# Optimization experiments

Measured on AMD Instinct MI355X. Metric: run time of the kernel, lower is better.

The kernel has to match this reference:

```python
import jax, jax.numpy as jnp
import numpy as np

N = 10000
E = 320000
F_IN = 512
NHID = 32
LATENT = 16


def setup_inputs() -> dict:
    key = jax.random.key(0)
    k1, k2, k3, k4, k5 = jax.random.split(key, 5)
    x = jax.random.normal(k1, (N, F_IN), dtype=jnp.float32)
    W1 = jax.random.normal(k2, (F_IN, NHID), dtype=jnp.float32) * (1.0 / np.sqrt(F_IN))
    W2 = jax.random.normal(k3, (NHID, LATENT), dtype=jnp.float32) * (1.0 / np.sqrt(NHID))
    edge_index = jax.random.randint(k4, (2, E), 0, N, dtype=jnp.int32)
    edge_weight = jax.random.uniform(k5, (E,), dtype=jnp.float32)
    return {"x": x, "W1": W1, "W2": W2, "edge_index": edge_index,
            "edge_weight": edge_weight}


def _spmm(edge_index, edge_weight, h):
    # out[dst] += w * h[src]  (sparse normalized-adjacency matmul)
    src, dst = edge_index[0], edge_index[1]
    msgs = edge_weight[:, None] * h[src]          # [E, D] gather + scale
    return jax.ops.segment_sum(msgs, dst, num_segments=N)  # [N, D]


def reference(x, W1, W2, edge_index, edge_weight):
    # GCNConv layer 1: adj @ (x @ W1)
    h = _spmm(edge_index, edge_weight, x @ W1)    # [N, NHID]
    # GCNConv layer 2: adj @ (h @ W2)
    z = _spmm(edge_index, edge_weight, h @ W2)    # [N, LATENT]
    # Inner-product decoder: sigmoid(z @ z^T)
    adj_recon = jax.nn.sigmoid(z @ z.T)           # [N, N]
    return adj_recon, z
```

## Files before the change

kernel.cpp:

```cpp
#include <hip/hip_runtime.h>
#include <cstdint>
#include <cstddef>

#define N_NODES 10000
#define F_IN    512
#define NHID    32
#define LATENT  16

__global__ __launch_bounds__(256) void gemm1_kernel(const float* __restrict__ x,
                                                    const float* __restrict__ W1,
                                                    float* __restrict__ h0) {
    __shared__ float xs[8][F_IN];
    const int row0 = blockIdx.x * 8;
    for (int t = threadIdx.x; t < 8 * F_IN; t += 256) {
        const int r = t >> 9;
        const int c = t & (F_IN - 1);
        if (row0 + r < N_NODES)
            xs[r][c] = x[(size_t)(row0 + r) * F_IN + c];
    }
    __syncthreads();

    const int col = threadIdx.x & 31;
    const int r   = threadIdx.x >> 5;
    if (row0 + r < N_NODES) {
        float acc = 0.f;
#pragma unroll 8
        for (int k = 0; k < F_IN; ++k) {
            acc += xs[r][k] * W1[k * NHID + col];
        }
        h0[(size_t)(row0 + r) * NHID + col] = acc;
    }
}

template <int D>
__global__ __launch_bounds__(256) void spmm_kernel(const int* __restrict__ src,
                                                   const int* __restrict__ dst,
                                                   const float* __restrict__ w,
                                                   const float* __restrict__ hin,
                                                   float* __restrict__ hout,
                                                   int E) {
    const int idx = blockIdx.x * 256 + threadIdx.x;
    const int e = idx / D;
    const int d = idx & (D - 1);
    if (e < E) {
        const int s = src[e];
        const int t = dst[e];
        const float val = w[e] * hin[(size_t)s * D + d];
        atomicAdd(&hout[(size_t)t * D + d], val);
    }
}

__global__ __launch_bounds__(256) void gemm2_kernel(const float* __restrict__ h,
                                                    const float* __restrict__ W2,
                                                    float* __restrict__ z0) {
    __shared__ float w2s[NHID * LATENT];
    for (int t = threadIdx.x; t < NHID * LATENT; t += 256) w2s[t] = W2[t];
    __syncthreads();

    const int idx = blockIdx.x * 256 + threadIdx.x;
    if (idx < N_NODES * LATENT) {
        const int row = idx >> 4;
        const int col = idx & (LATENT - 1);
        const float* __restrict__ hr = h + (size_t)row * NHID;
        float acc = 0.f;
#pragma unroll
        for (int k = 0; k < NHID; ++k) acc += hr[k] * w2s[k * LATENT + col];
        z0[idx] = acc;
    }
}

#define TI 32

__device__ __forceinline__ float sigmoid_fast(float x) {
    return __builtin_amdgcn_rcpf(1.0f + __expf(-x));
}

__global__ __launch_bounds__(256) void decoder_kernel(const float* __restrict__ z,
                                                      float* __restrict__ out) {
    const int j  = blockIdx.x * 256 + threadIdx.x;
    const int i0 = blockIdx.y * TI;

    float4 zj0, zj1, zj2, zj3;
    if (j < N_NODES) {
        const float4* __restrict__ zp = (const float4*)(z + (size_t)j * LATENT);
        zj0 = zp[0]; zj1 = zp[1]; zj2 = zp[2]; zj3 = zp[3];
    } else {
        zj0 = zj1 = zj2 = zj3 = make_float4(0.f, 0.f, 0.f, 0.f);
    }

    const int imax = min(TI, N_NODES - i0);
    if (imax == TI) {
#pragma unroll 4
        for (int ii = 0; ii < TI; ++ii) {
            const float4* __restrict__ zi = (const float4*)(z + (size_t)(i0 + ii) * LATENT);
            const float4 a0 = zi[0], a1 = zi[1], a2 = zi[2], a3 = zi[3];
            float acc = a0.x * zj0.x + a0.y * zj0.y + a0.z * zj0.z + a0.w * zj0.w
                      + a1.x * zj1.x + a1.y * zj1.y + a1.z * zj1.z + a1.w * zj1.w
                      + a2.x * zj2.x + a2.y * zj2.y + a2.z * zj2.z + a2.w * zj2.w
                      + a3.x * zj3.x + a3.y * zj3.y + a3.z * zj3.z + a3.w * zj3.w;
            if (j < N_NODES) {
                __builtin_nontemporal_store(sigmoid_fast(acc),
                                            &out[(size_t)(i0 + ii) * N_NODES + j]);
            }
        }
    } else {
        for (int ii = 0; ii < imax; ++ii) {
            const float4* __restrict__ zi = (const float4*)(z + (size_t)(i0 + ii) * LATENT);
            const float4 a0 = zi[0], a1 = zi[1], a2 = zi[2], a3 = zi[3];
            float acc = a0.x * zj0.x + a0.y * zj0.y + a0.z * zj0.z + a0.w * zj0.w
                      + a1.x * zj1.x + a1.y * zj1.y + a1.z * zj1.z + a1.w * zj1.w
                      + a2.x * zj2.x + a2.y * zj2.y + a2.z * zj2.z + a2.w * zj2.w
                      + a3.x * zj3.x + a3.y * zj3.y + a3.z * zj3.z + a3.w * zj3.w;
            if (j < N_NODES) {
                __builtin_nontemporal_store(sigmoid_fast(acc),
                                            &out[(size_t)(i0 + ii) * N_NODES + j]);
            }
        }
    }
}

extern "C" void kernel_launch(void* const* d_in, const int* in_sizes, int n_in,
                              void* d_out, int out_size, void* d_ws, size_t ws_size,
                              hipStream_t stream) {
    const float* x  = (const float*)d_in[0];
    const float* W1 = (const float*)d_in[1];
    const float* W2 = (const float*)d_in[2];
    const int*   ei = (const int*)d_in[3];
    const float* ew = (const float*)d_in[4];
    const int E = in_sizes[3] / 2;
    const int* src = ei;
    const int* dst = ei + E;

    float* out = (float*)d_out;
    float* z   = out + (size_t)N_NODES * N_NODES;

    float* h0 = out;
    float* h  = h0 + N_NODES * NHID;
    float* z0 = h  + N_NODES * NHID;

    hipMemsetAsync(h, 0, (size_t)N_NODES * NHID * sizeof(float), stream);
    hipMemsetAsync(z, 0, (size_t)N_NODES * LATENT * sizeof(float), stream);

    gemm1_kernel<<<(N_NODES + 7) / 8, 256, 0, stream>>>(x, W1, h0);
    spmm_kernel<NHID><<<(E * NHID + 255) / 256, 256, 0, stream>>>(src, dst, ew, h0, h, E);

    gemm2_kernel<<<(N_NODES * LATENT + 255) / 256, 256, 0, stream>>>(h, W2, z0);
    spmm_kernel<LATENT><<<(E * LATENT + 255) / 256, 256, 0, stream>>>(src, dst, ew, z0, z, E);

    dim3 dgrid((N_NODES + 255) / 256, (N_NODES + TI - 1) / TI);
    decoder_kernel<<<dgrid, 256, 0, stream>>>(z, out);
}
```

Before: 511.8 us.

## Build CSR by destination, replace atomic SpMM with gather, retune GEMMs and decoder

Adds a histogram, a single-block scan and a scatter pass that build a destination-sorted CSR of (src, weight) pairs on every call. Both SpMM layers become per-node gather reductions instead of per-edge atomicAdd scatters. Separately, gemm1 is restructured to stage W1 in shared memory and use float4 accumulation, gemm2 uses vectorized loads, and the decoder computes two columns per thread with TI=40 and 64-bit nontemporal stores. The CSR build adds extra kernels, atomics and a serial scan. Edges with the same destination are placed in nondeterministic order, so floating-point sums are not bitwise reproducible.

```diff
diff --git a/kernel.cpp b/kernel.cpp
--- a/kernel.cpp
+++ b/kernel.cpp
@@ -7,47 +7,133 @@
 #define NHID    32
 #define LATENT  16
 
+typedef float v2f __attribute__((ext_vector_type(2)));
+
+#define OF_H0   0
+#define OF_H    320000
+#define OF_Z0   640000
+#define OF_DEG  800000
+#define OF_RP   810240
+#define OF_CUR  820496
+#define OF_ESW  830752
+
+__global__ __launch_bounds__(256) void hist_kernel(const int* __restrict__ dst,
+                                                   int* __restrict__ deg, int E) {
+    const int e = blockIdx.x * 256 + threadIdx.x;
+    if (e < E) atomicAdd(&deg[dst[e]], 1);
+}
+
+__global__ __launch_bounds__(1024) void scan_kernel(const int* __restrict__ deg,
+                                                    int* __restrict__ row_ptr,
+                                                    int* __restrict__ cursor) {
+    __shared__ int sums[1024];
+    const int tid = threadIdx.x;
+    const int base = tid * 10;
+    int local[10];
+    int s = 0;
+#pragma unroll
+    for (int i = 0; i < 10; ++i) { local[i] = s; s += deg[base + i]; }
+    sums[tid] = s;
+    __syncthreads();
+    for (int off = 1; off < 1024; off <<= 1) {
+        int v = (tid >= off) ? sums[tid - off] : 0;
+        __syncthreads();
+        sums[tid] += v;
+        __syncthreads();
+    }
+    const int excl = (tid == 0) ? 0 : sums[tid - 1];
+#pragma unroll
+    for (int i = 0; i < 10; ++i) {
+        const int g = base + i;
+        if (g <= N_NODES) {
+            const int rp = excl + local[i];
+            row_ptr[g] = rp;
+            cursor[g]  = rp;
+        }
+    }
+}
+
+__global__ __launch_bounds__(256) void scatter_kernel(const int* __restrict__ src,
+                                                      const int* __restrict__ dst,
+                                                      const float* __restrict__ w,
+                                                      int* __restrict__ cursor,
+                                                      int2* __restrict__ esw, int E) {
+    const int e = blockIdx.x * 256 + threadIdx.x;
+    if (e < E) {
+        const int d = dst[e];
+        const int pos = atomicAdd(&cursor[d], 1);
+        esw[pos] = make_int2(src[e], __float_as_int(w[e]));
+    }
+}
+
+#define G1_KC 256
 __global__ __launch_bounds__(256) void gemm1_kernel(const float* __restrict__ x,
                                                     const float* __restrict__ W1,
                                                     float* __restrict__ h0) {
-    __shared__ float xs[8][F_IN];
-    const int row0 = blockIdx.x * 8;
-    for (int t = threadIdx.x; t < 8 * F_IN; t += 256) {
-        const int r = t >> 9;
-        const int c = t & (F_IN - 1);
-        if (row0 + r < N_NODES)
-            xs[r][c] = x[(size_t)(row0 + r) * F_IN + c];
-    }
-    __syncthreads();
-
-    const int col = threadIdx.x & 31;
-    const int r   = threadIdx.x >> 5;
-    if (row0 + r < N_NODES) {
-        float acc = 0.f;
-#pragma unroll 8
-        for (int k = 0; k < F_IN; ++k) {
-            acc += xs[r][k] * W1[k * NHID + col];
-        }
-        h0[(size_t)(row0 + r) * NHID + col] = acc;
+    __shared__ float w1s[G1_KC * NHID];
+    const int row0 = blockIdx.x * 32;
+    const int rp   = threadIdx.x >> 3;
+    const int cg   = (threadIdx.x & 7) * 4;
+    const int gr   = min(row0 + rp, N_NODES - 1);
+    const float4* __restrict__ xrow = (const float4*)(x + (size_t)gr * F_IN);
+
+    float4 acc = make_float4(0.f, 0.f, 0.f, 0.f);
+
+    for (int kc = 0; kc < F_IN; kc += G1_KC) {
+        {
+            const float4* __restrict__ wg = (const float4*)(W1 + (size_t)kc * NHID);
+            float4* __restrict__ ws4 = (float4*)w1s;
+            const int b = threadIdx.x * 8;
+#pragma unroll
+            for (int i = 0; i < 8; ++i) ws4[b + i] = wg[b + i];
+        }
+        __syncthreads();
+
+        const int k4base = kc >> 2;
+#pragma unroll 4
+        for (int kk4 = 0; kk4 < G1_KC / 4; ++kk4) {
+            const float4 xv = xrow[k4base + kk4];
+            const float4 w0 = *(const float4*)&w1s[(kk4 * 4 + 0) * NHID + cg];
+            const float4 w1 = *(const float4*)&w1s[(kk4 * 4 + 1) * NHID + cg];
+            const float4 w2 = *(const float4*)&w1s[(kk4 * 4 + 2) * NHID + cg];
+            const float4 w3 = *(const float4*)&w1s[(kk4 * 4 + 3) * NHID + cg];
+            acc.x += xv.x * w0.x + xv.y * w1.x + xv.z * w2.x + xv.w * w3.x;
+            acc.y += xv.x * w0.y + xv.y * w1.y + xv.z * w2.y + xv.w * w3.y;
+            acc.z += xv.x * w0.z + xv.y * w1.z + xv.z * w2.z + xv.w * w3.z;
+            acc.w += xv.x * w0.w + xv.y * w1.w + xv.z * w2.w + xv.w * w3.w;
+        }
+        __syncthreads();
+    }
+
+    if (row0 + rp < N_NODES) {
+        *(float4*)&h0[(size_t)(row0 + rp) * NHID + cg] = acc;
     }
 }
 
 template <int D>
-__global__ __launch_bounds__(256) void spmm_kernel(const int* __restrict__ src,
-                                                   const int* __restrict__ dst,
-                                                   const float* __restrict__ w,
-                                                   const float* __restrict__ hin,
-                                                   float* __restrict__ hout,
-                                                   int E) {
+__global__ __launch_bounds__(256) void gather_kernel(const int* __restrict__ row_ptr,
+                                                     const int2* __restrict__ esw,
+                                                     const float* __restrict__ hin,
+                                                     float* __restrict__ hout) {
     const int idx = blockIdx.x * 256 + threadIdx.x;
-    const int e = idx / D;
+    const int n = idx / D;
     const int d = idx & (D - 1);
-    if (e < E) {
-        const int s = src[e];
-        const int t = dst[e];
-        const float val = w[e] * hin[(size_t)s * D + d];
-        atomicAdd(&hout[(size_t)t * D + d], val);
-    }
+    if (n >= N_NODES) return;
+    const int beg = row_ptr[n];
+    const int end = row_ptr[n + 1];
+    float acc = 0.f;
+    int p = beg;
+    for (; p + 1 < end; p += 2) {
+        const int2 e0 = esw[p];
+        const int2 e1 = esw[p + 1];
+        acc += __int_as_float(e0.y) * hin[(size_t)e0.x * D + d];
+        acc += __int_as_float(e1.y) * hin[(size_t)e1.x * D + d];
+    }
+    if (p < end) {
+        const int2 e0 = esw[p];
+        acc += __int_as_float(e0.y) * hin[(size_t)e0.x * D + d];
+    }
+    hout[(size_t)n * D + d] = acc;
 }
 
 __global__ __launch_bounds__(256) void gemm2_kernel(const float* __restrict__ h,
@@ -61,15 +147,21 @@
     if (idx < N_NODES * LATENT) {
         const int row = idx >> 4;
         const int col = idx & (LATENT - 1);
-        const float* __restrict__ hr = h + (size_t)row * NHID;
+        const float4* __restrict__ hr = (const float4*)(h + (size_t)row * NHID);
         float acc = 0.f;
 #pragma unroll
-        for (int k = 0; k < NHID; ++k) acc += hr[k] * w2s[k * LATENT + col];
+        for (int k4 = 0; k4 < NHID / 4; ++k4) {
+            const float4 hv = hr[k4];
+            acc += hv.x * w2s[(k4 * 4 + 0) * LATENT + col]
+                 + hv.y * w2s[(k4 * 4 + 1) * LATENT + col]
+                 + hv.z * w2s[(k4 * 4 + 2) * LATENT + col]
+                 + hv.w * w2s[(k4 * 4 + 3) * LATENT + col];
+        }
         z0[idx] = acc;
     }
 }
 
-#define TI 32
+#define TI 40
 
 __device__ __forceinline__ float sigmoid_fast(float x) {
     return __builtin_amdgcn_rcpf(1.0f + __expf(-x));
@@ -77,44 +169,37 @@
 
 __global__ __launch_bounds__(256) void decoder_kernel(const float* __restrict__ z,
                                                       float* __restrict__ out) {
-    const int j  = blockIdx.x * 256 + threadIdx.x;
+    const int j0 = (blockIdx.x * 256 + threadIdx.x) * 2;
     const int i0 = blockIdx.y * TI;
 
-    float4 zj0, zj1, zj2, zj3;
-    if (j < N_NODES) {
-        const float4* __restrict__ zp = (const float4*)(z + (size_t)j * LATENT);
-        zj0 = zp[0]; zj1 = zp[1]; zj2 = zp[2]; zj3 = zp[3];
+    float4 a0, a1, a2, a3, b0, b1, b2, b3;
+    if (j0 < N_NODES) {
+        const float4* __restrict__ zp = (const float4*)(z + (size_t)j0 * LATENT);
+        a0 = zp[0]; a1 = zp[1]; a2 = zp[2]; a3 = zp[3];
+        b0 = zp[4]; b1 = zp[5]; b2 = zp[6]; b3 = zp[7];
     } else {
-        zj0 = zj1 = zj2 = zj3 = make_float4(0.f, 0.f, 0.f, 0.f);
-    }
-
-    const int imax = min(TI, N_NODES - i0);
-    if (imax == TI) {
+        a0 = a1 = a2 = a3 = make_float4(0.f, 0.f, 0.f, 0.f);
+        b0 = b1 = b2 = b3 = a0;
+    }
+
 #pragma unroll 4
-        for (int ii = 0; ii < TI; ++ii) {
-            const float4* __restrict__ zi = (const float4*)(z + (size_t)(i0 + ii) * LATENT);
-            const float4 a0 = zi[0], a1 = zi[1], a2 = zi[2], a3 = zi[3];
-            float acc = a0.x * zj0.x + a0.y * zj0.y + a0.z * zj0.z + a0.w * zj0.w
-                      + a1.x * zj1.x + a1.y * zj1.y + a1.z * zj1.z + a1.w * zj1.w
-                      + a2.x * zj2.x + a2.y * zj2.y + a2.z * zj2.z + a2.w * zj2.w
-                      + a3.x * zj3.x + a3.y * zj3.y + a3.z * zj3.z + a3.w * zj3.w;
-            if (j < N_NODES) {
-                __builtin_nontemporal_store(sigmoid_fast(acc),
-                                            &out[(size_t)(i0 + ii) * N_NODES + j]);
-            }
-        }
-    } else {
-        for (int ii = 0; ii < imax; ++ii) {
-            const float4* __restrict__ zi = (const float4*)(z + (size_t)(i0 + ii) * LATENT);
-            const float4 a0 = zi[0], a1 = zi[1], a2 = zi[2], a3 = zi[3];
-            float acc = a0.x * zj0.x + a0.y * zj0.y + a0.z * zj0.z + a0.w * zj0.w
-                      + a1.x * zj1.x + a1.y * zj1.y + a1.z * zj1.z + a1.w * zj1.w
-                      + a2.x * zj2.x + a2.y * zj2.y + a2.z * zj2.z + a2.w * zj2.w
-                      + a3.x * zj3.x + a3.y * zj3.y + a3.z * zj3.z + a3.w * zj3.w;
-            if (j < N_NODES) {
-                __builtin_nontemporal_store(sigmoid_fast(acc),
-                                            &out[(size_t)(i0 + ii) * N_NODES + j]);
-            }
+    for (int ii = 0; ii < TI; ++ii) {
+        const int i = i0 + ii;
+        const float4* __restrict__ zi = (const float4*)(z + (size_t)i * LATENT);
+        const float4 c0 = zi[0], c1 = zi[1], c2 = zi[2], c3 = zi[3];
+        const float s0 = c0.x * a0.x + c0.y * a0.y + c0.z * a0.z + c0.w * a0.w
+                       + c1.x * a1.x + c1.y * a1.y + c1.z * a1.z + c1.w * a1.w
+                       + c2.x * a2.x + c2.y * a2.y + c2.z * a2.z + c2.w * a2.w
+                       + c3.x * a3.x + c3.y * a3.y + c3.z * a3.z + c3.w * a3.w;
+        const float s1 = c0.x * b0.x + c0.y * b0.y + c0.z * b0.z + c0.w * b0.w
+                       + c1.x * b1.x + c1.y * b1.y + c1.z * b1.z + c1.w * b1.w
+                       + c2.x * b2.x + c2.y * b2.y + c2.z * b2.z + c2.w * b2.w
+                       + c3.x * b3.x + c3.y * b3.y + c3.z * b3.z + c3.w * b3.w;
+        if (j0 < N_NODES) {
+            v2f r;
+            r.x = sigmoid_fast(s0);
+            r.y = sigmoid_fast(s1);
+            __builtin_nontemporal_store(r, (v2f*)(out + (size_t)i * N_NODES + j0));
         }
     }
 }
@@ -134,19 +219,25 @@
     float* out = (float*)d_out;
     float* z   = out + (size_t)N_NODES * N_NODES;
 
-    float* h0 = out;
-    float* h  = h0 + N_NODES * NHID;
-    float* z0 = h  + N_NODES * NHID;
-
-    hipMemsetAsync(h, 0, (size_t)N_NODES * NHID * sizeof(float), stream);
-    hipMemsetAsync(z, 0, (size_t)N_NODES * LATENT * sizeof(float), stream);
-
-    gemm1_kernel<<<(N_NODES + 7) / 8, 256, 0, stream>>>(x, W1, h0);
-    spmm_kernel<NHID><<<(E * NHID + 255) / 256, 256, 0, stream>>>(src, dst, ew, h0, h, E);
+    float* h0     = out + OF_H0;
+    float* h      = out + OF_H;
+    float* z0     = out + OF_Z0;
+    int*   deg    = (int*)(out + OF_DEG);
+    int*   rowp   = (int*)(out + OF_RP);
+    int*   cursor = (int*)(out + OF_CUR);
+    int2*  esw    = (int2*)(out + OF_ESW);
+
+    hipMemsetAsync(deg, 0, 10240 * sizeof(int), stream);
+    hist_kernel<<<(E + 255) / 256, 256, 0, stream>>>(dst, deg, E);
+    scan_kernel<<<1, 1024, 0, stream>>>(deg, rowp, cursor);
+    scatter_kernel<<<(E + 255) / 256, 256, 0, stream>>>(src, dst, ew, cursor, esw, E);
+
+    gemm1_kernel<<<(N_NODES + 31) / 32, 256, 0, stream>>>(x, W1, h0);
+    gather_kernel<NHID><<<(N_NODES * NHID + 255) / 256, 256, 0, stream>>>(rowp, esw, h0, h);
 
     gemm2_kernel<<<(N_NODES * LATENT + 255) / 256, 256, 0, stream>>>(h, W2, z0);
-    spmm_kernel<LATENT><<<(E * LATENT + 255) / 256, 256, 0, stream>>>(src, dst, ew, z0, z, E);
-
-    dim3 dgrid((N_NODES + 255) / 256, (N_NODES + TI - 1) / TI);
+    gather_kernel<LATENT><<<(N_NODES * LATENT + 255) / 256, 256, 0, stream>>>(rowp, esw, z0, z);
+
+    dim3 dgrid((N_NODES / 2 + 255) / 256, N_NODES / TI);
     decoder_kernel<<<dgrid, 256, 0, stream>>>(z, out);
 }
```

After: 529.2 us. +3.4%, slower.

## Fuse memset into GEMM1, fuse GEMM2 into SpMM2, vectorize decoder stores

Applied to the files above, without the earlier changes.

The two memsets are folded into a combined stage-1 kernel that computes x@W1 with W1 staged in shared memory and float4 outputs, while extra blocks zero the accumulators. The second layer's dense projection is fused into the SpMM, so each edge computes h[src]@W2 on the fly. This removes the z0 buffer and a launch but repeats the 32x16 projection per edge. The decoder now computes 4 columns per thread with 128-bit nontemporal stores and TI=40, dropping the tail-handling branch. It relies on N being divisible by 4 and by 40.

```diff
diff --git a/kernel.cpp b/kernel.cpp
--- a/kernel.cpp
+++ b/kernel.cpp
@@ -7,69 +7,123 @@
 #define NHID    32
 #define LATENT  16
 
-__global__ __launch_bounds__(256) void gemm1_kernel(const float* __restrict__ x,
-                                                    const float* __restrict__ W1,
-                                                    float* __restrict__ h0) {
-    __shared__ float xs[8][F_IN];
-    const int row0 = blockIdx.x * 8;
-    for (int t = threadIdx.x; t < 8 * F_IN; t += 256) {
-        const int r = t >> 9;
-        const int c = t & (F_IN - 1);
-        if (row0 + r < N_NODES)
-            xs[r][c] = x[(size_t)(row0 + r) * F_IN + c];
+typedef float v4f __attribute__((ext_vector_type(4)));
+
+#define OF_H0   0
+#define OF_H    320000
+
+#define G1_TILES 313
+#define ZERO_BLOCKS 64
+#define G1_KC 256
+
+__global__ __launch_bounds__(256) void stage1_kernel(const float* __restrict__ x,
+                                                     const float* __restrict__ W1,
+                                                     float* __restrict__ h0,
+                                                     float* __restrict__ h,
+                                                     float* __restrict__ z) {
+    __shared__ float w1s[G1_KC * NHID];
+
+    if (blockIdx.x >= G1_TILES) {
+        const int tid = (blockIdx.x - G1_TILES) * 256 + threadIdx.x;
+        const int nthr = ZERO_BLOCKS * 256;
+        float4* __restrict__ h4 = (float4*)h;
+        float4* __restrict__ z4 = (float4*)z;
+        const v4f zero = {0.f, 0.f, 0.f, 0.f};
+        for (int i = tid; i < (N_NODES * NHID) / 4; i += nthr)
+            *(v4f*)&h4[i] = zero;
+        for (int i = tid; i < (N_NODES * LATENT) / 4; i += nthr)
+            *(v4f*)&z4[i] = zero;
+        return;
     }
-    __syncthreads();
 
-    const int col = threadIdx.x & 31;
-    const int r   = threadIdx.x >> 5;
-    if (row0 + r < N_NODES) {
-        float acc = 0.f;
-#pragma unroll 8
-        for (int k = 0; k < F_IN; ++k) {
-            acc += xs[r][k] * W1[k * NHID + col];
+    const int row0 = blockIdx.x * 32;
+    const int rp   = threadIdx.x >> 3;
+    const int cg   = (threadIdx.x & 7) * 4;
+    const int gr   = min(row0 + rp, N_NODES - 1);
+    const float4* __restrict__ xrow = (const float4*)(x + (size_t)gr * F_IN);
+
+    float4 acc = make_float4(0.f, 0.f, 0.f, 0.f);
+
+    for (int kc = 0; kc < F_IN; kc += G1_KC) {
+        {
+            const float4* __restrict__ wg = (const float4*)(W1 + (size_t)kc * NHID);
+            float4* __restrict__ ws4 = (float4*)w1s;
+            const int b = threadIdx.x * 8;
+#pragma unroll
+            for (int i = 0; i < 8; ++i) ws4[b + i] = wg[b + i];
         }
-        h0[(size_t)(row0 + r) * NHID + col] = acc;
+        __syncthreads();
+
+        const int k4base = kc >> 2;
+#pragma unroll 4
+        for (int kk4 = 0; kk4 < G1_KC / 4; ++kk4) {
+            const float4 xv = xrow[k4base + kk4];
+            const float4 w0 = *(const float4*)&w1s[(kk4 * 4 + 0) * NHID + cg];
+            const float4 w1 = *(const float4*)&w1s[(kk4 * 4 + 1) * NHID + cg];
+            const float4 w2 = *(const float4*)&w1s[(kk4 * 4 + 2) * NHID + cg];
+            const float4 w3 = *(const float4*)&w1s[(kk4 * 4 + 3) * NHID + cg];
+            acc.x += xv.x * w0.x + xv.y * w1.x + xv.z * w2.x + xv.w * w3.x;
+            acc.y += xv.x * w0.y + xv.y * w1.y + xv.z * w2.y + xv.w * w3.y;
+            acc.z += xv.x * w0.z + xv.y * w1.z + xv.z * w2.z + xv.w * w3.z;
+            acc.w += xv.x * w0.w + xv.y * w1.w + xv.z * w2.w + xv.w * w3.w;
+        }
+        __syncthreads();
+    }
+
+    if (row0 + rp < N_NODES) {
+        *(float4*)&h0[(size_t)(row0 + rp) * NHID + cg] = acc;
     }
 }
 
-template <int D>
-__global__ __launch_bounds__(256) void spmm_kernel(const int* __restrict__ src,
-                                                   const int* __restrict__ dst,
-                                                   const float* __restrict__ w,
-                                                   const float* __restrict__ hin,
-                                                   float* __restrict__ hout,
-                                                   int E) {
+__global__ __launch_bounds__(256) void spmm32_kernel(const int* __restrict__ src,
+                                                     const int* __restrict__ dst,
+                                                     const float* __restrict__ w,
+                                                     const float* __restrict__ hin,
+                                                     float* __restrict__ hout,
+                                                     int E) {
     const int idx = blockIdx.x * 256 + threadIdx.x;
-    const int e = idx / D;
-    const int d = idx & (D - 1);
+    const int e = idx >> 5;
+    const int d = idx & 31;
     if (e < E) {
         const int s = src[e];
         const int t = dst[e];
-        const float val = w[e] * hin[(size_t)s * D + d];
-        atomicAdd(&hout[(size_t)t * D + d], val);
+        const float val = w[e] * hin[(size_t)s * NHID + d];
+        atomicAdd(&hout[(size_t)t * NHID + d], val);
     }
 }
 
-__global__ __launch_bounds__(256) void gemm2_kernel(const float* __restrict__ h,
-                                                    const float* __restrict__ W2,
-                                                    float* __restrict__ z0) {
+__global__ __launch_bounds__(256) void l2_fused_kernel(const int* __restrict__ src,
+                                                       const int* __restrict__ dst,
+                                                       const float* __restrict__ w,
+                                                       const float* __restrict__ h,
+                                                       const float* __restrict__ W2,
+                                                       float* __restrict__ z,
+                                                       int E) {
     __shared__ float w2s[NHID * LATENT];
     for (int t = threadIdx.x; t < NHID * LATENT; t += 256) w2s[t] = W2[t];
     __syncthreads();
 
     const int idx = blockIdx.x * 256 + threadIdx.x;
-    if (idx < N_NODES * LATENT) {
-        const int row = idx >> 4;
-        const int col = idx & (LATENT - 1);
-        const float* __restrict__ hr = h + (size_t)row * NHID;
+    const int e = idx >> 4;
+    const int d = idx & (LATENT - 1);
+    if (e < E) {
+        const int s = src[e];
+        const int t = dst[e];
+        const float4* __restrict__ hr = (const float4*)(h + (size_t)s * NHID);
         float acc = 0.f;
 #pragma unroll
-        for (int k = 0; k < NHID; ++k) acc += hr[k] * w2s[k * LATENT + col];
-        z0[idx] = acc;
+        for (int k4 = 0; k4 < NHID / 4; ++k4) {
+            const float4 hv = hr[k4];
+            acc += hv.x * w2s[(k4 * 4 + 0) * LATENT + d]
+                 + hv.y * w2s[(k4 * 4 + 1) * LATENT + d]
+                 + hv.z * w2s[(k4 * 4 + 2) * LATENT + d]
+                 + hv.w * w2s[(k4 * 4 + 3) * LATENT + d];
+        }
+        atomicAdd(&z[(size_t)t * LATENT + d], w[e] * acc);
     }
 }
 
-#define TI 32
+#define TI 40
 
 __device__ __forceinline__ float sigmoid_fast(float x) {
     return __builtin_amdgcn_rcpf(1.0f + __expf(-x));
@@ -77,45 +131,35 @@
 
 __global__ __launch_bounds__(256) void decoder_kernel(const float* __restrict__ z,
                                                       float* __restrict__ out) {
-    const int j  = blockIdx.x * 256 + threadIdx.x;
+    const int j0 = (blockIdx.x * 256 + threadIdx.x) * 4;
     const int i0 = blockIdx.y * TI;
+    if (j0 >= N_NODES) return;
 
-    float4 zj0, zj1, zj2, zj3;
-    if (j < N_NODES) {
-        const float4* __restrict__ zp = (const float4*)(z + (size_t)j * LATENT);
-        zj0 = zp[0]; zj1 = zp[1]; zj2 = zp[2]; zj3 = zp[3];
-    } else {
-        zj0 = zj1 = zj2 = zj3 = make_float4(0.f, 0.f, 0.f, 0.f);
+    float4 zj[4][4];
+    {
+        const float4* __restrict__ zp = (const float4*)(z + (size_t)j0 * LATENT);
+#pragma unroll
+        for (int c = 0; c < 4; ++c)
+#pragma unroll
+            for (int q = 0; q < 4; ++q) zj[c][q] = zp[c * 4 + q];
     }
 
-    const int imax = min(TI, N_NODES - i0);
-    if (imax == TI) {
-#pragma unroll 4
-        for (int ii = 0; ii < TI; ++ii) {
-            const float4* __restrict__ zi = (const float4*)(z + (size_t)(i0 + ii) * LATENT);
-            const float4 a0 = zi[0], a1 = zi[1], a2 = zi[2], a3 = zi[3];
-            float acc = a0.x * zj0.x + a0.y * zj0.y + a0.z * zj0.z + a0.w * zj0.w
-                      + a1.x * zj1.x + a1.y * zj1.y + a1.z * zj1.z + a1.w * zj1.w
-                      + a2.x * zj2.x + a2.y * zj2.y + a2.z * zj2.z + a2.w * zj2.w
-                      + a3.x * zj3.x + a3.y * zj3.y + a3.z * zj3.z + a3.w * zj3.w;
-            if (j < N_NODES) {
-                __builtin_nontemporal_store(sigmoid_fast(acc),
-                                            &out[(size_t)(i0 + ii) * N_NODES + j]);
-            }
+#pragma unroll 2
+    for (int ii = 0; ii < TI; ++ii) {
+        const int i = i0 + ii;
+        const float4* __restrict__ zi = (const float4*)(z + (size_t)i * LATENT);
+        const float4 c0 = zi[0], c1 = zi[1], c2 = zi[2], c3 = zi[3];
+        v4f r;
+#pragma unroll
+        for (int c = 0; c < 4; ++c) {
+            const float s =
+                  c0.x * zj[c][0].x + c0.y * zj[c][0].y + c0.z * zj[c][0].z + c0.w * zj[c][0].w
+                + c1.x * zj[c][1].x + c1.y * zj[c][1].y + c1.z * zj[c][1].z + c1.w * zj[c][1].w
+                + c2.x * zj[c][2].x + c2.y * zj[c][2].y + c2.z * zj[c][2].z + c2.w * zj[c][2].w
+                + c3.x * zj[c][3].x + c3.y * zj[c][3].y + c3.z * zj[c][3].z + c3.w * zj[c][3].w;
+            r[c] = sigmoid_fast(s);
         }
-    } else {
-        for (int ii = 0; ii < imax; ++ii) {
-            const float4* __restrict__ zi = (const float4*)(z + (size_t)(i0 + ii) * LATENT);
-            const float4 a0 = zi[0], a1 = zi[1], a2 = zi[2], a3 = zi[3];
-            float acc = a0.x * zj0.x + a0.y * zj0.y + a0.z * zj0.z + a0.w * zj0.w
-                      + a1.x * zj1.x + a1.y * zj1.y + a1.z * zj1.z + a1.w * zj1.w
-                      + a2.x * zj2.x + a2.y * zj2.y + a2.z * zj2.z + a2.w * zj2.w
-                      + a3.x * zj3.x + a3.y * zj3.y + a3.z * zj3.z + a3.w * zj3.w;
-            if (j < N_NODES) {
-                __builtin_nontemporal_store(sigmoid_fast(acc),
-                                            &out[(size_t)(i0 + ii) * N_NODES + j]);
-            }
-        }
+        __builtin_nontemporal_store(r, (v4f*)(out + (size_t)i * N_NODES + j0));
     }
 }
 
@@ -133,20 +177,15 @@
 
     float* out = (float*)d_out;
     float* z   = out + (size_t)N_NODES * N_NODES;
+    float* h0  = out + OF_H0;
+    float* h   = out + OF_H;
 
-    float* h0 = out;
-    float* h  = h0 + N_NODES * NHID;
-    float* z0 = h  + N_NODES * NHID;
+    stage1_kernel<<<G1_TILES + ZERO_BLOCKS, 256, 0, stream>>>(x, W1, h0, h, z);
 
-    hipMemsetAsync(h, 0, (size_t)N_NODES * NHID * sizeof(float), stream);
-    hipMemsetAsync(z, 0, (size_t)N_NODES * LATENT * sizeof(float), stream);
+    spmm32_kernel<<<(E * NHID + 255) / 256, 256, 0, stream>>>(src, dst, ew, h0, h, E);
 
-    gemm1_kernel<<<(N_NODES + 7) / 8, 256, 0, stream>>>(x, W1, h0);
-    spmm_kernel<NHID><<<(E * NHID + 255) / 256, 256, 0, stream>>>(src, dst, ew, h0, h, E);
+    l2_fused_kernel<<<(E * LATENT + 255) / 256, 256, 0, stream>>>(src, dst, ew, h, W2, z, E);
 
-    gemm2_kernel<<<(N_NODES * LATENT + 255) / 256, 256, 0, stream>>>(h, W2, z0);
-    spmm_kernel<LATENT><<<(E * LATENT + 255) / 256, 256, 0, stream>>>(src, dst, ew, z0, z, E);
-
-    dim3 dgrid((N_NODES + 255) / 256, (N_NODES + TI - 1) / TI);
+    dim3 dgrid((N_NODES / 4 + 255) / 256, N_NODES / TI);
     decoder_kernel<<<dgrid, 256, 0, stream>>>(z, out);
 }
```

Measured after the change: 512.0 us. About the same (+0.0%).
